# Performance work log

Hardware: AMD Instinct MI355X
Metric: run time of the kernel (lower is better)

## Reference

```python
import math
import jax, jax.numpy as jnp
import numpy as np

B, T, D = 1, 4096, 1024
NH, NKV, HD = 16, 4, 64          # nhead, n_kv_heads, head_dim
WINDOW = 256


def _alibi_slopes(nhead: int) -> np.ndarray:
    closest_pow2 = 2 ** math.floor(math.log2(nhead))
    base = 2.0 ** (-2.0 ** (-(math.log2(closest_pow2) - 3)))
    slopes = base ** np.arange(1, closest_pow2 + 1, dtype=np.float32)
    if closest_pow2 < nhead:
        extra_base = 2.0 ** (-2.0 ** (-(math.log2(2 * closest_pow2) - 3)))
        extra = extra_base ** np.arange(1, 2 * (nhead - closest_pow2) + 1, 2, dtype=np.float32)
        slopes = np.concatenate([slopes, extra])
    return slopes.astype(np.float32)


def setup_inputs() -> dict:
    key = jax.random.key(0)
    ks = jax.random.split(key, 9)
    s = 0.02
    return {
        "x": jax.random.normal(ks[0], (B, T, D), jnp.float32),
        "Wq": jax.random.normal(ks[1], (D, NH * HD), jnp.float32) * s,
        "bq": jax.random.normal(ks[2], (NH * HD,), jnp.float32) * s,
        "Wk": jax.random.normal(ks[3], (D, NKV * HD), jnp.float32) * s,
        "bk": jax.random.normal(ks[4], (NKV * HD,), jnp.float32) * s,
        "Wv": jax.random.normal(ks[5], (D, NKV * HD), jnp.float32) * s,
        "bv": jax.random.normal(ks[6], (NKV * HD,), jnp.float32) * s,
        "Wo": jax.random.normal(ks[7], (D, D), jnp.float32) * s,
        "bo": jax.random.normal(ks[8], (D,), jnp.float32) * s,
    }


def _attn_bias():
    # ALiBi bias + causal + sliding-window mask, shape (NH, T, T)
    pos = jnp.arange(T)
    dist = pos[None, :] - pos[:, None]          # col - row; <=0 where causal-allowed
    allowed = (dist <= 0) & (-dist < WINDOW)    # causal AND within window
    slopes = jnp.asarray(_alibi_slopes(NH))     # (NH,)
    bias = -slopes[:, None, None] * jnp.abs(dist)[None].astype(jnp.float32)
    return jnp.where(allowed[None], bias, -jnp.inf)  # (NH, T, T)


def reference(x, Wq, bq, Wk, bk, Wv, bv, Wo, bo):
    q = (x @ Wq + bq).reshape(B, T, NH, HD).transpose(0, 2, 1, 3)   # (B,NH,T,HD)
    k = (x @ Wk + bk).reshape(B, T, NKV, HD).transpose(0, 2, 1, 3)  # (B,NKV,T,HD)
    v = (x @ Wv + bv).reshape(B, T, NKV, HD).transpose(0, 2, 1, 3)
    # GQA: repeat_interleave kv heads to NH
    k = jnp.repeat(k, NH // NKV, axis=1)
    v = jnp.repeat(v, NH // NKV, axis=1)
    scale = 1.0 / math.sqrt(HD)
    scores = jnp.einsum("bhtd,bhsd->bhts", q, k) * scale + _attn_bias()[None]
    probs = jax.nn.softmax(scores, axis=-1)
    out = jnp.einsum("bhts,bhsd->bhtd", probs, v)        # (B,NH,T,HD)
    out = out.transpose(0, 2, 1, 3).reshape(B, T, D)
    return out @ Wo + bo
```

## Files before the change

kernel.cpp:

```cpp
#include <hip/hip_runtime.h>

typedef __bf16 bf16;
typedef __bf16 bf16x4 __attribute__((ext_vector_type(4)));
typedef __bf16 bf16x8 __attribute__((ext_vector_type(8)));
typedef float f32x4 __attribute__((ext_vector_type(4)));

#define T_LEN   4096
#define D_MODEL 1024
#define QKV_LD  1536
#define VT_LD   4128
#define WINDOW  256

__device__ __forceinline__ void gload_lds16(const bf16* g, bf16* l) {
    __builtin_amdgcn_global_load_lds((const __attribute__((address_space(1))) void*)g,
                                     (__attribute__((address_space(3))) void*)l, 16, 0, 0);
}


__global__ __launch_bounds__(256) void prep_fused(
    const float* __restrict__ x,
    const float* __restrict__ Wq, const float* __restrict__ Wk,
    const float* __restrict__ Wv, const float* __restrict__ Wo,
    bf16* __restrict__ xb, bf16* __restrict__ WtQKV, bf16* __restrict__ WtO)
{
    __shared__ float t[32][33];
    const int blk = blockIdx.x;
    if (blk < 2048) {
        int i = (blk * 256 + threadIdx.x) * 8;
        float4 a = *(const float4*)(x + i);
        float4 b = *(const float4*)(x + i + 4);
        bf16x8 o;
        o[0] = (bf16)a.x; o[1] = (bf16)a.y; o[2] = (bf16)a.z; o[3] = (bf16)a.w;
        o[4] = (bf16)b.x; o[5] = (bf16)b.y; o[6] = (bf16)b.z; o[7] = (bf16)b.w;
        *(bf16x8*)(xb + i) = o;
        return;
    }
    const float* W; bf16* Wt; int n0, k0, Ns, nofs;
    if (blk < 3584) {
        int b = blk - 2048;
        n0 = (b % 48) * 32; k0 = (b / 48) * 32;
        if (n0 < 1024)      { W = Wq; Ns = 1024; nofs = 0; }
        else if (n0 < 1280) { W = Wk; Ns = 256;  nofs = 1024; }
        else                { W = Wv; Ns = 256;  nofs = 1280; }
        Wt = WtQKV;
    } else {
        int b = blk - 3584;
        n0 = (b % 32) * 32; k0 = (b / 32) * 32;
        W = Wo; Ns = 1024; nofs = 0; Wt = WtO;
    }
    int tx = threadIdx.x & 31, ty = threadIdx.x >> 5;
#pragma unroll
    for (int it = 0; it < 4; ++it)
        t[ty + it * 8][tx] = W[(size_t)(k0 + ty + it * 8) * Ns + (n0 - nofs) + tx];
    __syncthreads();
#pragma unroll
    for (int it = 0; it < 4; ++it)
        Wt[(size_t)(n0 + ty + it * 8) * 1024 + k0 + tx] = (bf16)t[tx][ty + it * 8];
}


template <bool OUT_BF16, bool QKV_BIAS>
__global__ __launch_bounds__(256) void gemm_bt(
    const bf16* __restrict__ A, const bf16* __restrict__ Bt,
    const float* __restrict__ b0, const float* __restrict__ b1,
    const float* __restrict__ b2, void* __restrict__ Cv, bf16* __restrict__ Vt,
    int M, int N, int K, int nbx, int bands_per_xcd)
{
    __shared__ bf16 As[128 * 32];
    __shared__ bf16 Bs[64 * 32];
    const int blk = blockIdx.x;
    const int xcd = blk & 7;
    const int s   = blk >> 3;
    const int m0 = (xcd * bands_per_xcd + s / nbx) * 128;
    const int n0 = (s % nbx) * 64;
    const int tid  = threadIdx.x;
    const int wave = tid >> 6, lane = tid & 63;
    const int quad = lane >> 4, l16 = lane & 15;
    const int wm = wave >> 1, wn = wave & 1;

    f32x4 acc[4][2] = {};

    const int srow = wave * 16 + (lane >> 2);
    const int scol = (lane & 3) * 8;
    const bf16* ga0 = A  + (size_t)(m0 + srow) * K + scol;
    const bf16* ga1 = A  + (size_t)(m0 + srow + 64) * K + scol;
    const bf16* gb  = Bt + (size_t)(n0 + srow) * K + scol;
    bf16* la0 = As + srow * 32 + scol;
    bf16* la1 = As + (srow + 64) * 32 + scol;
    bf16* lb  = Bs + srow * 32 + scol;

    const int nk = K >> 5;
    for (int kt = 0; kt < nk; ++kt) {
        __syncthreads();
        gload_lds16(ga0 + kt * 32, la0);
        gload_lds16(ga1 + kt * 32, la1);
        gload_lds16(gb  + kt * 32, lb);
        __syncthreads();
        bf16x8 af[4], bfr[2];
#pragma unroll
        for (int i = 0; i < 4; ++i)
            af[i] = *(const bf16x8*)&As[(wm * 64 + i * 16 + l16) * 32 + quad * 8];
#pragma unroll
        for (int j = 0; j < 2; ++j)
            bfr[j] = *(const bf16x8*)&Bs[(wn * 32 + j * 16 + l16) * 32 + quad * 8];
#pragma unroll
        for (int i = 0; i < 4; ++i)
#pragma unroll
            for (int j = 0; j < 2; ++j)
                acc[i][j] = __builtin_amdgcn_mfma_f32_16x16x32_bf16(af[i], bfr[j], acc[i][j], 0, 0, 0);
    }

    const bool vtile = QKV_BIAS && (n0 >= 1280);
#pragma unroll
    for (int i = 0; i < 4; ++i)
#pragma unroll
        for (int j = 0; j < 2; ++j) {
            const int col = n0 + wn * 32 + j * 16 + l16;
            const float bb = QKV_BIAS
                ? (col < 1024 ? b0[col] : (col < 1280 ? b1[col - 1024] : b2[col - 1280]))
                : b0[col];
            const int row0 = m0 + wm * 64 + i * 16 + quad * 4;
            if (vtile) {
                bf16x4 pv;
#pragma unroll
                for (int r = 0; r < 4; ++r) pv[r] = (bf16)(acc[i][j][r] + bb);
                *(bf16x4*)&Vt[(size_t)(col - 1280) * VT_LD + row0] = pv;
            } else {
#pragma unroll
                for (int r = 0; r < 4; ++r) {
                    const float v = acc[i][j][r] + bb;
                    if (OUT_BF16) ((bf16*)Cv)[(size_t)(row0 + r) * N + col] = (bf16)v;
                    else          ((float*)Cv)[(size_t)(row0 + r) * N + col] = v;
                }
            }
        }
}


__global__ __launch_bounds__(256) void attn_kernel(
    const bf16* __restrict__ QKV, const bf16* __restrict__ Vt, bf16* __restrict__ Oa)
{
    __shared__ bf16 Ps[4][16][296];
    const int wave = threadIdx.x >> 6;
    const int lane = threadIdx.x & 63;
    const int q0 = (blockIdx.x * 4 + wave) * 16;
    const int h  = blockIdx.y;
    const int kh = h >> 2;
    const int quad = lane >> 4, l16 = lane & 15;
    const float slope = exp2f(-0.5f * (float)(h + 1));
    const int lo = (q0 >= 256) ? (q0 - 256) : 0;

    const bf16* qp = QKV + (size_t)(q0 + l16) * QKV_LD + h * 64 + quad * 8;
    bf16x8 qf0 = *(const bf16x8*)qp;
    bf16x8 qf1 = *(const bf16x8*)(qp + 32);

    f32x4 s[17];
#pragma unroll
    for (int t = 0; t < 17; ++t) {
        const bf16* kp = QKV + (size_t)(lo + t * 16 + l16) * QKV_LD + D_MODEL + kh * 64 + quad * 8;
        bf16x8 kf0 = *(const bf16x8*)kp;
        bf16x8 kf1 = *(const bf16x8*)(kp + 32);
        f32x4 a = {};
        a = __builtin_amdgcn_mfma_f32_16x16x32_bf16(qf0, kf0, a, 0, 0, 0);
        a = __builtin_amdgcn_mfma_f32_16x16x32_bf16(qf1, kf1, a, 0, 0, 0);
        s[t] = a;
    }

    float rinv[4];
#pragma unroll
    for (int r = 0; r < 4; ++r) {
        const int row = q0 + quad * 4 + r;
        float mx = -1e30f;
#pragma unroll
        for (int t = 0; t < 17; ++t) {
            const int key = lo + t * 16 + l16;
            float v = s[t][r] * 0.125f - slope * (float)(row - key);
            const bool ok = (key <= row) && (key > row - WINDOW);
            v = ok ? v : -1e30f;
            s[t][r] = v;
            mx = fmaxf(mx, v);
        }
#pragma unroll
        for (int d = 1; d < 16; d <<= 1) mx = fmaxf(mx, __shfl_xor(mx, d));
        float sum = 0.f;
#pragma unroll
        for (int t = 0; t < 17; ++t) {
            float p = __expf(s[t][r] - mx);
            s[t][r] = p;
            sum += p;
        }
#pragma unroll
        for (int d = 1; d < 16; d <<= 1) sum += __shfl_xor(sum, d);
        rinv[r] = 1.f / sum;
    }

    {
        int idx = lane;
#pragma unroll
        for (int it = 0; it < 4; ++it) {
            Ps[wave][(idx >> 4) & 15][272 + (idx & 15)] = (bf16)0.f;
            idx += 64;
        }
    }
#pragma unroll
    for (int t = 0; t < 17; ++t)
#pragma unroll
        for (int r = 0; r < 4; ++r)
            Ps[wave][quad * 4 + r][t * 16 + l16] = (bf16)(s[t][r] * rinv[r]);
    __syncthreads();

    f32x4 o[4] = {};
#pragma unroll
    for (int c = 0; c < 9; ++c) {
        bf16x8 pf = *(const bf16x8*)&Ps[wave][l16][c * 32 + quad * 8];
#pragma unroll
        for (int j = 0; j < 4; ++j) {
            const bf16* vp = Vt + (size_t)(kh * 64 + j * 16 + l16) * VT_LD + lo + c * 32 + quad * 8;
            bf16x8 vf = *(const bf16x8*)vp;
            o[j] = __builtin_amdgcn_mfma_f32_16x16x32_bf16(pf, vf, o[j], 0, 0, 0);
        }
    }

#pragma unroll
    for (int j = 0; j < 4; ++j)
#pragma unroll
        for (int r = 0; r < 4; ++r)
            Oa[(size_t)(q0 + quad * 4 + r) * D_MODEL + h * 64 + j * 16 + l16] = (bf16)o[j][r];
}


extern "C" void kernel_launch(void* const* d_in, const int* in_sizes, int n_in,
                              void* d_out, int out_size, void* d_ws, size_t ws_size,
                              hipStream_t stream) {
    const float* x  = (const float*)d_in[0];
    const float* Wq = (const float*)d_in[1];
    const float* bq = (const float*)d_in[2];
    const float* Wk = (const float*)d_in[3];
    const float* bk = (const float*)d_in[4];
    const float* Wv = (const float*)d_in[5];
    const float* bv = (const float*)d_in[6];
    const float* Wo = (const float*)d_in[7];
    const float* bo = (const float*)d_in[8];
    float* out = (float*)d_out;

    char* ws = (char*)d_ws;
    bf16*  xb    = (bf16*)(ws);
    bf16*  WtQKV = (bf16*)(ws + 8388608);
    bf16*  WtO   = (bf16*)(ws + 11534336);
    bf16*  QKV   = (bf16*)(ws + 13637632);
    bf16*  Vt    = (bf16*)(ws + 26220544);
    bf16*  AO    = (bf16*)(ws + 28334080);

    prep_fused<<<4608, 256, 0, stream>>>(x, Wq, Wk, Wv, Wo, xb, WtQKV, WtO);

    gemm_bt<true, true><<<768, 256, 0, stream>>>(
        xb, WtQKV, bq, bk, bv, QKV, Vt, 4096, 1536, 1024, 24, 4);

    attn_kernel<<<dim3(64, 16), 256, 0, stream>>>(QKV, Vt, AO);

    gemm_bt<false, false><<<512, 256, 0, stream>>>(
        AO, WtO, bo, nullptr, nullptr, out, nullptr, 4096, 1024, 1024, 16, 4);
}
```

Before: 172.9 us.

## Triple-buffer GEMM LDS tiles with async global-to-LDS prefetch two steps ahead

```diff
diff --git a/kernel.cpp b/kernel.cpp
--- a/kernel.cpp
+++ b/kernel.cpp
@@ -66,8 +66,8 @@
     const float* __restrict__ b2, void* __restrict__ Cv, bf16* __restrict__ Vt,
     int M, int N, int K, int nbx, int bands_per_xcd)
 {
-    __shared__ bf16 As[128 * 32];
-    __shared__ bf16 Bs[64 * 32];
+    __shared__ bf16 As[3][128 * 32];
+    __shared__ bf16 Bs[3][64 * 32];
     const int blk = blockIdx.x;
     const int xcd = blk & 7;
     const int s   = blk >> 3;
@@ -85,29 +85,48 @@
     const bf16* ga0 = A  + (size_t)(m0 + srow) * K + scol;
     const bf16* ga1 = A  + (size_t)(m0 + srow + 64) * K + scol;
     const bf16* gb  = Bt + (size_t)(n0 + srow) * K + scol;
-    bf16* la0 = As + srow * 32 + scol;
-    bf16* la1 = As + (srow + 64) * 32 + scol;
-    bf16* lb  = Bs + srow * 32 + scol;
+    const int sA0 = srow * 32 + scol;
+    const int sA1 = (srow + 64) * 32 + scol;
+    const int sB  = srow * 32 + scol;
+
+    bf16 *Ac = &As[0][0], *An = &As[1][0], *Ao = &As[2][0];
+    bf16 *Bc = &Bs[0][0], *Bn = &Bs[1][0], *Bo = &Bs[2][0];
+
+    gload_lds16(ga0, Ac + sA0);
+    gload_lds16(ga1, Ac + sA1);
+    gload_lds16(gb,  Bc + sB);
+    gload_lds16(ga0 + 32, An + sA0);
+    gload_lds16(ga1 + 32, An + sA1);
+    gload_lds16(gb  + 32, Bn + sB);
+
+    const int raoff = (wm * 64 + l16) * 32 + quad * 8;
+    const int rboff = (wn * 32 + l16) * 32 + quad * 8;
 
     const int nk = K >> 5;
     for (int kt = 0; kt < nk; ++kt) {
-        __syncthreads();
-        gload_lds16(ga0 + kt * 32, la0);
-        gload_lds16(ga1 + kt * 32, la1);
-        gload_lds16(gb  + kt * 32, lb);
-        __syncthreads();
+        if (kt + 1 < nk) asm volatile("s_waitcnt vmcnt(3)" ::: "memory");
+        else             asm volatile("s_waitcnt vmcnt(0)" ::: "memory");
+        asm volatile("s_barrier" ::: "memory");
+        if (kt + 2 < nk) {
+            gload_lds16(ga0 + (kt + 2) * 32, Ao + sA0);
+            gload_lds16(ga1 + (kt + 2) * 32, Ao + sA1);
+            gload_lds16(gb  + (kt + 2) * 32, Bo + sB);
+        }
         bf16x8 af[4], bfr[2];
 #pragma unroll
         for (int i = 0; i < 4; ++i)
-            af[i] = *(const bf16x8*)&As[(wm * 64 + i * 16 + l16) * 32 + quad * 8];
+            af[i] = *(const bf16x8*)(Ac + raoff + i * 16 * 32);
 #pragma unroll
         for (int j = 0; j < 2; ++j)
-            bfr[j] = *(const bf16x8*)&Bs[(wn * 32 + j * 16 + l16) * 32 + quad * 8];
+            bfr[j] = *(const bf16x8*)(Bc + rboff + j * 16 * 32);
 #pragma unroll
         for (int i = 0; i < 4; ++i)
 #pragma unroll
             for (int j = 0; j < 2; ++j)
                 acc[i][j] = __builtin_amdgcn_mfma_f32_16x16x32_bf16(af[i], bfr[j], acc[i][j], 0, 0, 0);
+        bf16* t;
+        t = Ac; Ac = An; An = Ao; Ao = t;
+        t = Bc; Bc = Bn; Bn = Bo; Bo = t;
     }
 
     const bool vtile = QKV_BIAS && (n0 >= 1280);
```

New measurement: 172.1 us. About the same (-0.4%).

## Replace LDS-staged GEMM with direct-register double-buffered loads and 128x128 tiles

Applied to the files above, without the earlier changes.

```diff
diff --git a/kernel.cpp b/kernel.cpp
--- a/kernel.cpp
+++ b/kernel.cpp
@@ -8,13 +8,9 @@
 #define T_LEN   4096
 #define D_MODEL 1024
 #define QKV_LD  1536
+#define KDIM    1024
 #define VT_LD   4128
 #define WINDOW  256
-
-__device__ __forceinline__ void gload_lds16(const bf16* g, bf16* l) {
-    __builtin_amdgcn_global_load_lds((const __attribute__((address_space(1))) void*)g,
-                                     (__attribute__((address_space(3))) void*)l, 16, 0, 0);
-}
 
 
 __global__ __launch_bounds__(256) void prep_fused(
@@ -64,58 +60,54 @@
     const bf16* __restrict__ A, const bf16* __restrict__ Bt,
     const float* __restrict__ b0, const float* __restrict__ b1,
     const float* __restrict__ b2, void* __restrict__ Cv, bf16* __restrict__ Vt,
-    int M, int N, int K, int nbx, int bands_per_xcd)
+    int M, int N, int nbx, int bands_per_xcd)
 {
-    __shared__ bf16 As[128 * 32];
-    __shared__ bf16 Bs[64 * 32];
     const int blk = blockIdx.x;
     const int xcd = blk & 7;
     const int s   = blk >> 3;
     const int m0 = (xcd * bands_per_xcd + s / nbx) * 128;
-    const int n0 = (s % nbx) * 64;
+    const int n0 = (s % nbx) * 128;
     const int tid  = threadIdx.x;
     const int wave = tid >> 6, lane = tid & 63;
     const int quad = lane >> 4, l16 = lane & 15;
     const int wm = wave >> 1, wn = wave & 1;
 
-    f32x4 acc[4][2] = {};
-
-    const int srow = wave * 16 + (lane >> 2);
-    const int scol = (lane & 3) * 8;
-    const bf16* ga0 = A  + (size_t)(m0 + srow) * K + scol;
-    const bf16* ga1 = A  + (size_t)(m0 + srow + 64) * K + scol;
-    const bf16* gb  = Bt + (size_t)(n0 + srow) * K + scol;
-    bf16* la0 = As + srow * 32 + scol;
-    bf16* la1 = As + (srow + 64) * 32 + scol;
-    bf16* lb  = Bs + srow * 32 + scol;
-
-    const int nk = K >> 5;
+    f32x4 acc[4][4] = {};
+
+    const bf16* pa = A  + (size_t)(m0 + wm * 64 + l16) * KDIM + quad * 8;
+    const bf16* pb = Bt + (size_t)(n0 + wn * 64 + l16) * KDIM + quad * 8;
+
+    bf16x8 af[2][4], bfr[2][4];
+#pragma unroll
+    for (int i = 0; i < 4; ++i) {
+        af[0][i]  = *(const bf16x8*)(pa + i * 16 * KDIM);
+        bfr[0][i] = *(const bf16x8*)(pb + i * 16 * KDIM);
+    }
+
+    const int nk = KDIM / 32;
+#pragma unroll
     for (int kt = 0; kt < nk; ++kt) {
-        __syncthreads();
-        gload_lds16(ga0 + kt * 32, la0);
-        gload_lds16(ga1 + kt * 32, la1);
-        gload_lds16(gb  + kt * 32, lb);
-        __syncthreads();
-        bf16x8 af[4], bfr[2];
+        const int cur = kt & 1, nxt = cur ^ 1;
+        if (kt + 1 < nk) {
+#pragma unroll
+            for (int i = 0; i < 4; ++i) {
+                af[nxt][i]  = *(const bf16x8*)(pa + i * 16 * KDIM + (kt + 1) * 32);
+                bfr[nxt][i] = *(const bf16x8*)(pb + i * 16 * KDIM + (kt + 1) * 32);
+            }
+        }
 #pragma unroll
         for (int i = 0; i < 4; ++i)
-            af[i] = *(const bf16x8*)&As[(wm * 64 + i * 16 + l16) * 32 + quad * 8];
-#pragma unroll
-        for (int j = 0; j < 2; ++j)
-            bfr[j] = *(const bf16x8*)&Bs[(wn * 32 + j * 16 + l16) * 32 + quad * 8];
-#pragma unroll
-        for (int i = 0; i < 4; ++i)
-#pragma unroll
-            for (int j = 0; j < 2; ++j)
-                acc[i][j] = __builtin_amdgcn_mfma_f32_16x16x32_bf16(af[i], bfr[j], acc[i][j], 0, 0, 0);
+#pragma unroll
+            for (int j = 0; j < 4; ++j)
+                acc[i][j] = __builtin_amdgcn_mfma_f32_16x16x32_bf16(af[cur][i], bfr[cur][j], acc[i][j], 0, 0, 0);
     }
 
     const bool vtile = QKV_BIAS && (n0 >= 1280);
 #pragma unroll
     for (int i = 0; i < 4; ++i)
 #pragma unroll
-        for (int j = 0; j < 2; ++j) {
-            const int col = n0 + wn * 32 + j * 16 + l16;
+        for (int j = 0; j < 4; ++j) {
+            const int col = n0 + wn * 64 + j * 16 + l16;
             const float bb = QKV_BIAS
                 ? (col < 1024 ? b0[col] : (col < 1280 ? b1[col - 1024] : b2[col - 1280]))
                 : b0[col];
@@ -253,11 +245,11 @@
 
     prep_fused<<<4608, 256, 0, stream>>>(x, Wq, Wk, Wv, Wo, xb, WtQKV, WtO);
 
-    gemm_bt<true, true><<<768, 256, 0, stream>>>(
-        xb, WtQKV, bq, bk, bv, QKV, Vt, 4096, 1536, 1024, 24, 4);
+    gemm_bt<true, true><<<384, 256, 0, stream>>>(
+        xb, WtQKV, bq, bk, bv, QKV, Vt, 4096, 1536, 12, 4);
 
     attn_kernel<<<dim3(64, 16), 256, 0, stream>>>(QKV, Vt, AO);
 
-    gemm_bt<false, false><<<512, 256, 0, stream>>>(
-        AO, WtO, bo, nullptr, nullptr, out, nullptr, 4096, 1024, 1024, 16, 4);
-}
+    gemm_bt<false, false><<<256, 256, 0, stream>>>(
+        AO, WtO, bo, nullptr, nullptr, out, nullptr, 4096, 1024, 8, 4);
+}
```

After: 228.0 us. 31.8% more time.

## Triple-buffer GEMM LDS loads and shrink tiles to 64x64 with two waves

Applied to the files above, without the earlier changes.

```diff
diff --git a/kernel.cpp b/kernel.cpp
--- a/kernel.cpp
+++ b/kernel.cpp
@@ -60,54 +60,73 @@
 
 
 template <bool OUT_BF16, bool QKV_BIAS>
-__global__ __launch_bounds__(256) void gemm_bt(
+__global__ __launch_bounds__(128) void gemm_bt(
     const bf16* __restrict__ A, const bf16* __restrict__ Bt,
     const float* __restrict__ b0, const float* __restrict__ b1,
     const float* __restrict__ b2, void* __restrict__ Cv, bf16* __restrict__ Vt,
     int M, int N, int K, int nbx, int bands_per_xcd)
 {
-    __shared__ bf16 As[128 * 32];
-    __shared__ bf16 Bs[64 * 32];
+    __shared__ bf16 As[3][64 * 32];
+    __shared__ bf16 Bs[3][64 * 32];
     const int blk = blockIdx.x;
     const int xcd = blk & 7;
     const int s   = blk >> 3;
-    const int m0 = (xcd * bands_per_xcd + s / nbx) * 128;
+    const int m0 = (xcd * bands_per_xcd + s / nbx) * 64;
     const int n0 = (s % nbx) * 64;
     const int tid  = threadIdx.x;
-    const int wave = tid >> 6, lane = tid & 63;
+    const int w    = tid >> 6, lane = tid & 63;
     const int quad = lane >> 4, l16 = lane & 15;
-    const int wm = wave >> 1, wn = wave & 1;
 
     f32x4 acc[4][2] = {};
 
-    const int srow = wave * 16 + (lane >> 2);
-    const int scol = (lane & 3) * 8;
-    const bf16* ga0 = A  + (size_t)(m0 + srow) * K + scol;
-    const bf16* ga1 = A  + (size_t)(m0 + srow + 64) * K + scol;
-    const bf16* gb  = Bt + (size_t)(n0 + srow) * K + scol;
-    bf16* la0 = As + srow * 32 + scol;
-    bf16* la1 = As + (srow + 64) * 32 + scol;
-    bf16* lb  = Bs + srow * 32 + scol;
+    const int segA0 = w * 128 + lane;
+    const int segA1 = w * 128 + 64 + lane;
+    const bf16* gA0 = A  + (size_t)(m0 + (segA0 >> 2)) * K + (segA0 & 3) * 8;
+    const bf16* gA1 = A  + (size_t)(m0 + (segA1 >> 2)) * K + (segA1 & 3) * 8;
+    const bf16* gB0 = Bt + (size_t)(n0 + (segA0 >> 2)) * K + (segA0 & 3) * 8;
+    const bf16* gB1 = Bt + (size_t)(n0 + (segA1 >> 2)) * K + (segA1 & 3) * 8;
+    const int dA0 = segA0 * 8, dA1 = segA1 * 8;
+
+    int bc = 0, bn = 1, bo = 2;
+
+    gload_lds16(gA0,      &As[0][0] + dA0);
+    gload_lds16(gA1,      &As[0][0] + dA1);
+    gload_lds16(gB0,      &Bs[0][0] + dA0);
+    gload_lds16(gB1,      &Bs[0][0] + dA1);
+    gload_lds16(gA0 + 32, &As[1][0] + dA0);
+    gload_lds16(gA1 + 32, &As[1][0] + dA1);
+    gload_lds16(gB0 + 32, &Bs[1][0] + dA0);
+    gload_lds16(gB1 + 32, &Bs[1][0] + dA1);
+
+    const int raoff = l16 * 32 + quad * 8;
+    const int rboff = (w * 32 + l16) * 32 + quad * 8;
 
     const int nk = K >> 5;
     for (int kt = 0; kt < nk; ++kt) {
-        __syncthreads();
-        gload_lds16(ga0 + kt * 32, la0);
-        gload_lds16(ga1 + kt * 32, la1);
-        gload_lds16(gb  + kt * 32, lb);
-        __syncthreads();
+        if (kt + 1 < nk) asm volatile("s_waitcnt vmcnt(4)" ::: "memory");
+        else             asm volatile("s_waitcnt vmcnt(0)" ::: "memory");
+        asm volatile("s_barrier" ::: "memory");
+        if (kt + 2 < nk) {
+            gload_lds16(gA0 + (kt + 2) * 32, &As[bo][0] + dA0);
+            gload_lds16(gA1 + (kt + 2) * 32, &As[bo][0] + dA1);
+            gload_lds16(gB0 + (kt + 2) * 32, &Bs[bo][0] + dA0);
+            gload_lds16(gB1 + (kt + 2) * 32, &Bs[bo][0] + dA1);
+        }
+        const bf16* Ac = &As[bc][0];
+        const bf16* Bc = &Bs[bc][0];
         bf16x8 af[4], bfr[2];
 #pragma unroll
         for (int i = 0; i < 4; ++i)
-            af[i] = *(const bf16x8*)&As[(wm * 64 + i * 16 + l16) * 32 + quad * 8];
+            af[i] = *(const bf16x8*)(Ac + raoff + i * 16 * 32);
 #pragma unroll
         for (int j = 0; j < 2; ++j)
-            bfr[j] = *(const bf16x8*)&Bs[(wn * 32 + j * 16 + l16) * 32 + quad * 8];
+            bfr[j] = *(const bf16x8*)(Bc + rboff + j * 16 * 32);
 #pragma unroll
         for (int i = 0; i < 4; ++i)
 #pragma unroll
             for (int j = 0; j < 2; ++j)
                 acc[i][j] = __builtin_amdgcn_mfma_f32_16x16x32_bf16(af[i], bfr[j], acc[i][j], 0, 0, 0);
+        int t = bc; bc = bn; bn = bo; bo = t;
     }
 
     const bool vtile = QKV_BIAS && (n0 >= 1280);
@@ -115,11 +134,11 @@
     for (int i = 0; i < 4; ++i)
 #pragma unroll
         for (int j = 0; j < 2; ++j) {
-            const int col = n0 + wn * 32 + j * 16 + l16;
+            const int col = n0 + w * 32 + j * 16 + l16;
             const float bb = QKV_BIAS
                 ? (col < 1024 ? b0[col] : (col < 1280 ? b1[col - 1024] : b2[col - 1280]))
                 : b0[col];
-            const int row0 = m0 + wm * 64 + i * 16 + quad * 4;
+            const int row0 = m0 + i * 16 + quad * 4;
             if (vtile) {
                 bf16x4 pv;
 #pragma unroll
@@ -253,11 +272,11 @@
 
     prep_fused<<<4608, 256, 0, stream>>>(x, Wq, Wk, Wv, Wo, xb, WtQKV, WtO);
 
-    gemm_bt<true, true><<<768, 256, 0, stream>>>(
-        xb, WtQKV, bq, bk, bv, QKV, Vt, 4096, 1536, 1024, 24, 4);
+    gemm_bt<true, true><<<1536, 128, 0, stream>>>(
+        xb, WtQKV, bq, bk, bv, QKV, Vt, 4096, 1536, 1024, 24, 8);
 
     attn_kernel<<<dim3(64, 16), 256, 0, stream>>>(QKV, Vt, AO);
 
-    gemm_bt<false, false><<<512, 256, 0, stream>>>(
-        AO, WtO, bo, nullptr, nullptr, out, nullptr, 4096, 1024, 1024, 16, 4);
-}
+    gemm_bt<false, false><<<1024, 128, 0, stream>>>(
+        AO, WtO, bo, nullptr, nullptr, out, nullptr, 4096, 1024, 1024, 16, 8);
+}
```

After: 173.2 us (median of 2 runs). No clear change (+0.2%).
